# Kernel optimization log

Hardware: AMD Instinct MI355X
Metric: run time of the kernel (lower is better)

Reference implementation:

```python
import jax, jax.numpy as jnp
import numpy as np

NUM_INPUTS = 1024
NUM_HIDDEN = 1024
FORGET_GATE_BIAS = -1.0
EPS = 1e-5


def layer_norm_1d(x, weight, bias):
    # Matches torch LayerNorm1D: std is unbiased (ddof=1), divide by (std + eps)
    mean = jnp.mean(x, axis=1, keepdims=True)
    std = jnp.std(x, axis=1, keepdims=True, ddof=1)
    return (x - mean) / (std + EPS) * weight + bias


def setup_inputs() -> dict:
    key = jax.random.key(0)
    ks = jax.random.split(key, 8)
    B, I, H = 4096, NUM_INPUTS, NUM_HIDDEN
    lim_i = 1.0 / np.sqrt(I)
    lim_h = 1.0 / np.sqrt(H)
    return {
        "inputs": jax.random.normal(ks[0], (B, I), jnp.float32),
        "hx": jax.random.normal(ks[1], (B, H), jnp.float32),
        "cx": jax.random.normal(ks[2], (B, H), jnp.float32),
        "w_i2h": jax.random.uniform(ks[3], (4 * H, I), jnp.float32, -lim_i, lim_i),
        "b_i2h": jax.random.uniform(ks[4], (4 * H,), jnp.float32, -lim_i, lim_i),
        "w_h2h": jax.random.uniform(ks[5], (4 * H, H), jnp.float32, -lim_h, lim_h),
        "b_h2h": jax.random.uniform(ks[6], (4 * H,), jnp.float32, -lim_h, lim_h),
        "ln_i2h_w": jnp.ones((1, 4 * H), jnp.float32),
        "ln_i2h_b": jnp.zeros((1, 4 * H), jnp.float32),
        "ln_h2h_w": jnp.ones((1, 4 * H), jnp.float32),
        "ln_h2h_b": jnp.zeros((1, 4 * H), jnp.float32),
        "ln_h2o_w": jnp.ones((1, H), jnp.float32),
        "ln_h2o_b": jnp.zeros((1, H), jnp.float32),
    }


def reference(inputs, hx, cx, w_i2h, b_i2h, w_h2h, b_h2h,
              ln_i2h_w, ln_i2h_b, ln_h2h_w, ln_h2h_b, ln_h2o_w, ln_h2o_b):
    H = NUM_HIDDEN
    i2h = inputs @ w_i2h.T + b_i2h          # [B, 4H]
    h2h = hx @ w_h2h.T + b_h2h              # [B, 4H]
    x = layer_norm_1d(i2h, ln_i2h_w, ln_i2h_b) + layer_norm_1d(h2h, ln_h2h_w, ln_h2h_b)
    g_i, g_f, g_o, g_c = jnp.split(x, 4, axis=1)
    in_gate = jax.nn.sigmoid(g_i)
    forget_gate = jax.nn.sigmoid(g_f + FORGET_GATE_BIAS)
    out_gate = jax.nn.sigmoid(g_o)
    in_transform = jnp.tanh(g_c)
    cx_new = forget_gate * cx + in_gate * in_transform
    hx_new = out_gate * jnp.tanh(layer_norm_1d(cx_new, ln_h2o_w, ln_h2o_b))
    return hx_new, cx_new
```

## Files before the change

kernel.cpp:

```cpp
#include <hip/hip_runtime.h>
#include <hip/hip_bf16.h>
#include <math.h>

#define NI 1024
#define NH 1024
#define H4 4096
#define FGB (-1.0f)
#define LN_EPS 1e-5f
#define NKT 32

typedef unsigned short u16;
typedef __attribute__((ext_vector_type(8))) short short8;
typedef __attribute__((ext_vector_type(8))) unsigned short ushort8v;
typedef __attribute__((ext_vector_type(16))) float f32x16;

__device__ __forceinline__ float bf2f(u16 u) {
    union { unsigned int i; float f; } v; v.i = ((unsigned int)u) << 16; return v.f;
}
__device__ __forceinline__ u16 f2bf(float f) {
    __hip_bfloat16 h = __float2bfloat16(f);
    return __builtin_bit_cast(u16, h);
}
__device__ __forceinline__ float fast_sigmoid(float x) {
    return 1.0f / (1.0f + __expf(-x));
}
__device__ __forceinline__ float fast_tanh(float x) {
    return 1.0f - 2.0f / (__expf(2.0f * x) + 1.0f);
}

__device__ __forceinline__ void gload16(const u16* g, u16* l) {
    __builtin_amdgcn_global_load_lds(
        (const __attribute__((address_space(1))) void*)g,
        (__attribute__((address_space(3))) void*)l,
        16, 0, 0);
}

__global__ __launch_bounds__(256) void shuffle_cast(
    const float* __restrict__ a, const float* __restrict__ b,
    const float* __restrict__ c, const float* __restrict__ d,
    u16* __restrict__ oa, u16* __restrict__ ob,
    u16* __restrict__ oc, u16* __restrict__ od)
{
    __shared__ u16 sT[32][264];

    const int my = blockIdx.y;
    const float* src = (my == 0) ? a : (my == 1) ? b : (my == 2) ? c : d;
    u16*         dst = (my == 0) ? oa : (my == 1) ? ob : (my == 2) ? oc : od;

    const int mtile = blockIdx.x >> 2;
    const int slab  = blockIdx.x & 3;
    const int t     = threadIdx.x;
    const int w     = t >> 6;
    const int lane  = t & 63;

    const float* s0 = src + (size_t)(mtile * 32) * 1024 + slab * 256 + lane * 4;
#pragma unroll
    for (int i = 0; i < 8; ++i) {
        const int row = i * 4 + w;
        float4 v = *(const float4*)(s0 + (size_t)row * 1024);
        ushort4 pk;
        pk.x = f2bf(v.x); pk.y = f2bf(v.y); pk.z = f2bf(v.z); pk.w = f2bf(v.w);
        *(ushort4*)&sT[row][lane * 4] = pk;
    }
    __syncthreads();

    const int r  = lane & 31;
    const int hi = lane >> 5;
#pragma unroll
    for (int j = 0; j < 2; ++j) {
        const int ktl = w * 2 + j;
        const int kt  = slab * 8 + ktl;
        u16* o = dst + ((size_t)(mtile * 32 + kt)) * 1024 + lane * 8;
#pragma unroll
        for (int kh = 0; kh < 2; ++kh) {
            ushort8v vv = *(const ushort8v*)&sT[r][ktl * 32 + kh * 16 + hi * 8];
            *(ushort8v*)(o + kh * 512) = vv;
        }
    }
}

__global__ __launch_bounds__(512, 2) void gemm_lds(
    const u16* __restrict__ Af0, const u16* __restrict__ Wf0,
    const float* __restrict__ bias0, u16* __restrict__ C0,
    const u16* __restrict__ Af1, const u16* __restrict__ Wf1,
    const float* __restrict__ bias1, u16* __restrict__ C1,
    int N)
{
    const u16*   Af   = blockIdx.z ? Af1 : Af0;
    const u16*   Wf   = blockIdx.z ? Wf1 : Wf0;
    const float* bias = blockIdx.z ? bias1 : bias0;
    u16*         C    = blockIdx.z ? C1 : C0;

    __shared__ __align__(16) u16 sA[4][8][2][512];
    __shared__ __align__(16) u16 sB[4][8][2][512];

    const int tid  = threadIdx.x;
    const int lane = tid & 63;
    const int wave = tid >> 6;
    const int wm   = wave >> 2;
    const int wn   = wave & 3;

    const u16* gA = Af + (size_t)(blockIdx.y * 8 + wave) * 32768 + lane * 8;
    const u16* gB = Wf + (size_t)(blockIdx.x * 8 + wave) * 32768 + lane * 8;

    f32x16 acc[4][2];
#pragma unroll
    for (int i = 0; i < 4; ++i)
#pragma unroll
        for (int j = 0; j < 2; ++j)
#pragma unroll
            for (int r = 0; r < 16; ++r)
                acc[i][j][r] = 0.f;

#define STAGE(kt)                                                            \
    do {                                                                     \
        gload16(gA + (size_t)(kt) * 1024,       &sA[(kt) & 3][wave][0][0]);  \
        gload16(gA + (size_t)(kt) * 1024 + 512, &sA[(kt) & 3][wave][1][0]);  \
        gload16(gB + (size_t)(kt) * 1024,       &sB[(kt) & 3][wave][0][0]);  \
        gload16(gB + (size_t)(kt) * 1024 + 512, &sB[(kt) & 3][wave][1][0]);  \
    } while (0)

    ushort8v a0_0, a1_0, a2_0, a3_0, b0_0, b1_0;
    ushort8v a0_1, a1_1, a2_1, a3_1, b0_1, b1_1;

#define R0(slot)                                                             \
    do {                                                                     \
        a0_0 = *(const ushort8v*)&sA[slot][wm * 4 + 0][0][lane * 8];         \
        b0_0 = *(const ushort8v*)&sB[slot][wn * 2 + 0][0][lane * 8];         \
        a1_0 = *(const ushort8v*)&sA[slot][wm * 4 + 1][0][lane * 8];         \
        b1_0 = *(const ushort8v*)&sB[slot][wn * 2 + 1][0][lane * 8];         \
        a2_0 = *(const ushort8v*)&sA[slot][wm * 4 + 2][0][lane * 8];         \
        a3_0 = *(const ushort8v*)&sA[slot][wm * 4 + 3][0][lane * 8];         \
    } while (0)
#define R1(slot)                                                             \
    do {                                                                     \
        a0_1 = *(const ushort8v*)&sA[slot][wm * 4 + 0][1][lane * 8];         \
        b0_1 = *(const ushort8v*)&sB[slot][wn * 2 + 0][1][lane * 8];         \
        a1_1 = *(const ushort8v*)&sA[slot][wm * 4 + 1][1][lane * 8];         \
        b1_1 = *(const ushort8v*)&sB[slot][wn * 2 + 1][1][lane * 8];         \
        a2_1 = *(const ushort8v*)&sA[slot][wm * 4 + 2][1][lane * 8];         \
        a3_1 = *(const ushort8v*)&sA[slot][wm * 4 + 3][1][lane * 8];         \
    } while (0)

#define MM(i, j, aa, bb) \
    acc[i][j] = __builtin_amdgcn_mfma_f32_32x32x16_bf16((short8)aa, (short8)bb, acc[i][j], 0, 0, 0)

#define M8(s)                                                                \
    do {                                                                     \
        __builtin_amdgcn_s_setprio(1);                                       \
        MM(0, 0, a0_##s, b0_##s); MM(1, 0, a1_##s, b0_##s);                  \
        MM(0, 1, a0_##s, b1_##s); MM(1, 1, a1_##s, b1_##s);                  \
        MM(2, 0, a2_##s, b0_##s); MM(3, 0, a3_##s, b0_##s);                  \
        MM(2, 1, a2_##s, b1_##s); MM(3, 1, a3_##s, b1_##s);                  \
        __builtin_amdgcn_s_setprio(0);                                       \
    } while (0)

#define FENCE() asm volatile("" ::: "memory")
#define WIN_TOP(kt)                                                          \
    do {                                                                     \
        if ((kt) == NKT - 1) {                                               \
            asm volatile("s_waitcnt vmcnt(0)" ::: "memory");                 \
        } else {                                                             \
            asm volatile("s_waitcnt vmcnt(4)" ::: "memory");                 \
        }                                                                    \
        FENCE();                                                             \
        __builtin_amdgcn_s_barrier();                                        \
        FENCE();                                                             \
        if ((kt) + 2 < NKT) STAGE((kt) + 2);                                 \
    } while (0)

    STAGE(0);
    STAGE(1);
    asm volatile("s_waitcnt vmcnt(4)" ::: "memory");
    FENCE();
    __builtin_amdgcn_s_barrier();
    FENCE();
    STAGE(2);
    R0(0);
    R1(0);
    M8(0);

    if ((wave & 1) == 0) {
#pragma unroll
        for (int kt = 1; kt < NKT; ++kt) {
            const int slot = kt & 3;
            WIN_TOP(kt);
            R0(slot);
            M8(1);
            R1(slot);
            M8(0);
        }
    } else {
#pragma unroll
        for (int kt = 1; kt < NKT; ++kt) {
            const int slot = kt & 3;
            WIN_TOP(kt);
            M8(1);
            __builtin_amdgcn_sched_barrier(0);
            R0(slot);
            R1(slot);
            M8(0);
        }
    }
    M8(1);

#undef STAGE
#undef R0
#undef R1
#undef MM
#undef M8
#undef WIN_TOP
#undef FENCE

    const int m0  = blockIdx.y * 256;
    const int n0  = blockIdx.x * 256;
    const int l31 = lane & 31;
    float bv[2];
#pragma unroll
    for (int tn = 0; tn < 2; ++tn)
        bv[tn] = bias[n0 + wn * 64 + tn * 32 + l31];

    const int rbase = (lane >> 5) * 4;
#pragma unroll
    for (int tm = 0; tm < 4; ++tm)
#pragma unroll
        for (int reg = 0; reg < 16; ++reg) {
            const int row = m0 + wm * 128 + tm * 32 + (reg & 3) + 8 * (reg >> 2) + rbase;
#pragma unroll
            for (int tn = 0; tn < 2; ++tn) {
                const int col = n0 + wn * 64 + tn * 32 + l31;
                C[(size_t)row * N + col] = f2bf(acc[tm][tn][reg] + bv[tn]);
            }
        }
}

__global__ __launch_bounds__(256) void lstm_pointwise(
    const u16* __restrict__ i2h, const u16* __restrict__ h2h,
    const float* __restrict__ cx,
    const float* __restrict__ lwx, const float* __restrict__ lbx,
    const float* __restrict__ lwy, const float* __restrict__ lby,
    const float* __restrict__ lwc, const float* __restrict__ lbc,
    float* __restrict__ hx_out, float* __restrict__ cx_out)
{
    __shared__ float red[16];

    const int row  = blockIdx.x;
    const int tid  = threadIdx.x;
    const int lane = tid & 63;
    const int wid  = tid >> 6;
    const int j0   = tid * 4;

    const u16* xr = i2h + (size_t)row * H4;
    const u16* yr = h2h + (size_t)row * H4;

    float xf[4][4], yf[4][4];
    float sx = 0.f, sxx = 0.f, sy = 0.f, syy = 0.f;
#pragma unroll
    for (int g = 0; g < 4; ++g) {
        ushort4 xv = *(const ushort4*)(xr + g * NH + j0);
        ushort4 yv = *(const ushort4*)(yr + g * NH + j0);
        xf[g][0] = bf2f(xv.x); xf[g][1] = bf2f(xv.y);
        xf[g][2] = bf2f(xv.z); xf[g][3] = bf2f(xv.w);
        yf[g][0] = bf2f(yv.x); yf[g][1] = bf2f(yv.y);
        yf[g][2] = bf2f(yv.z); yf[g][3] = bf2f(yv.w);
#pragma unroll
        for (int e = 0; e < 4; ++e) {
            sx += xf[g][e]; sxx += xf[g][e] * xf[g][e];
            sy += yf[g][e]; syy += yf[g][e] * yf[g][e];
        }
    }
#pragma unroll
    for (int m = 32; m; m >>= 1) {
        sx  += __shfl_xor(sx,  m, 64);
        sxx += __shfl_xor(sxx, m, 64);
        sy  += __shfl_xor(sy,  m, 64);
        syy += __shfl_xor(syy, m, 64);
    }
    if (lane == 0) {
        red[wid] = sx; red[4 + wid] = sxx; red[8 + wid] = sy; red[12 + wid] = syy;
    }
    __syncthreads();
    const float tsx  = red[0] + red[1] + red[2] + red[3];
    const float tsxx = red[4] + red[5] + red[6] + red[7];
    const float tsy  = red[8] + red[9] + red[10] + red[11];
    const float tsyy = red[12] + red[13] + red[14] + red[15];

    const float n1  = (float)H4;
    const float mx  = tsx / n1;
    const float ivx = 1.0f / (sqrtf(fmaxf((tsxx - tsx * tsx / n1) / (n1 - 1.f), 0.f)) + LN_EPS);
    const float my  = tsy / n1;
    const float ivy = 1.0f / (sqrtf(fmaxf((tsyy - tsy * tsy / n1) / (n1 - 1.f), 0.f)) + LN_EPS);

    float gate[4][4];
#pragma unroll
    for (int g = 0; g < 4; ++g) {
        float4 wxv = *(const float4*)(lwx + g * NH + j0);
        float4 bxv = *(const float4*)(lbx + g * NH + j0);
        float4 wyv = *(const float4*)(lwy + g * NH + j0);
        float4 byv = *(const float4*)(lby + g * NH + j0);
        gate[g][0] = (xf[g][0] - mx) * ivx * wxv.x + bxv.x + (yf[g][0] - my) * ivy * wyv.x + byv.x;
        gate[g][1] = (xf[g][1] - mx) * ivx * wxv.y + bxv.y + (yf[g][1] - my) * ivy * wyv.y + byv.y;
        gate[g][2] = (xf[g][2] - mx) * ivx * wxv.z + bxv.z + (yf[g][2] - my) * ivy * wyv.z + byv.z;
        gate[g][3] = (xf[g][3] - mx) * ivx * wxv.w + bxv.w + (yf[g][3] - my) * ivy * wyv.w + byv.w;
    }

    float4 cxv = *(const float4*)(cx + (size_t)row * NH + j0);
    const float cin[4] = {cxv.x, cxv.y, cxv.z, cxv.w};
    float cvl[4], og[4];
    float sc = 0.f, scc = 0.f;
#pragma unroll
    for (int e = 0; e < 4; ++e) {
        float ing = fast_sigmoid(gate[0][e]);
        float fg  = fast_sigmoid(gate[1][e] + FGB);
        og[e]     = fast_sigmoid(gate[2][e]);
        float tr  = fast_tanh(gate[3][e]);
        float c   = fg * cin[e] + ing * tr;
        cvl[e] = c; sc += c; scc += c * c;
    }
    *(float4*)(cx_out + (size_t)row * NH + j0) = make_float4(cvl[0], cvl[1], cvl[2], cvl[3]);

#pragma unroll
    for (int m = 32; m; m >>= 1) {
        sc  += __shfl_xor(sc,  m, 64);
        scc += __shfl_xor(scc, m, 64);
    }
    __syncthreads();
    if (lane == 0) { red[wid] = sc; red[4 + wid] = scc; }
    __syncthreads();
    const float tsc  = red[0] + red[1] + red[2] + red[3];
    const float tscc = red[4] + red[5] + red[6] + red[7];

    const float nc  = (float)NH;
    const float mc  = tsc / nc;
    const float ivc = 1.0f / (sqrtf(fmaxf((tscc - tsc * tsc / nc) / (nc - 1.f), 0.f)) + LN_EPS);

    float4 wcv = *(const float4*)(lwc + j0);
    float4 bcv = *(const float4*)(lbc + j0);
    float h0 = og[0] * fast_tanh((cvl[0] - mc) * ivc * wcv.x + bcv.x);
    float h1 = og[1] * fast_tanh((cvl[1] - mc) * ivc * wcv.y + bcv.y);
    float h2 = og[2] * fast_tanh((cvl[2] - mc) * ivc * wcv.z + bcv.z);
    float h3 = og[3] * fast_tanh((cvl[3] - mc) * ivc * wcv.w + bcv.w);
    *(float4*)(hx_out + (size_t)row * NH + j0) = make_float4(h0, h1, h2, h3);
}

extern "C" void kernel_launch(void* const* d_in, const int* in_sizes, int n_in,
                              void* d_out, int out_size, void* d_ws, size_t ws_size,
                              hipStream_t stream) {
    const float* inputs = (const float*)d_in[0];
    const float* hx     = (const float*)d_in[1];
    const float* cx     = (const float*)d_in[2];
    const float* w_i2h  = (const float*)d_in[3];
    const float* b_i2h  = (const float*)d_in[4];
    const float* w_h2h  = (const float*)d_in[5];
    const float* b_h2h  = (const float*)d_in[6];
    const float* lwx    = (const float*)d_in[7];
    const float* lbx    = (const float*)d_in[8];
    const float* lwy    = (const float*)d_in[9];
    const float* lby    = (const float*)d_in[10];
    const float* lwc    = (const float*)d_in[11];
    const float* lbc    = (const float*)d_in[12];

    const int B = in_sizes[0] / NI;

    u16* a_fr   = (u16*)d_ws;
    u16* hx_fr  = a_fr   + (size_t)B * NI;
    u16* wi_fr  = hx_fr  + (size_t)B * NH;
    u16* wh_fr  = wi_fr  + (size_t)H4 * NI;
    u16* i2h_bf = wh_fr  + (size_t)H4 * NH;
    u16* h2h_bf = i2h_bf + (size_t)B * H4;

    float* hx_out = (float*)d_out;
    float* cx_out = hx_out + (size_t)B * NH;

    shuffle_cast<<<dim3(512, 4), dim3(256), 0, stream>>>(
        inputs, hx, w_i2h, w_h2h, a_fr, hx_fr, wi_fr, wh_fr);

    gemm_lds<<<dim3(H4 / 256, B / 256, 2), dim3(512), 0, stream>>>(
        a_fr, wi_fr, b_i2h, i2h_bf,
        hx_fr, wh_fr, b_h2h, h2h_bf,
        H4);

    lstm_pointwise<<<dim3(B), dim3(256), 0, stream>>>(
        i2h_bf, h2h_bf, cx, lwx, lbx, lwy, lby, lwc, lbc, hx_out, cx_out);
}
```

Measured before the change: 237.6 us.

## Restructure GEMM main loop into double-buffered 64-wide K tiles with per-subslice staging

Replaces the 4-slot ring of 32-wide K tiles with a 2-slot buffer of 64-wide K tiles split into four sub-slices. Each sub-slice phase waits on its own load, barriers, reads its fragments, issues the prefetch for the same sub-slice of the next tile, then runs the MFMAs. It also drops the wave-parity split scheduling and the double fragment registers. The aim is finer-grained overlap of global loads with compute and lower register pressure, at the cost of one barrier per 16-wide K step instead of one per 32.

```diff
diff --git a/kernel.cpp b/kernel.cpp
--- a/kernel.cpp
+++ b/kernel.cpp
@@ -8,6 +8,7 @@
 #define FGB (-1.0f)
 #define LN_EPS 1e-5f
 #define NKT 32
+#define NT64 16
 
 typedef unsigned short u16;
 typedef __attribute__((ext_vector_type(8))) short short8;
@@ -91,8 +92,8 @@
     const float* bias = blockIdx.z ? bias1 : bias0;
     u16*         C    = blockIdx.z ? C1 : C0;
 
-    __shared__ __align__(16) u16 sA[4][8][2][512];
-    __shared__ __align__(16) u16 sB[4][8][2][512];
+    __shared__ __align__(16) u16 sA[2][8][4][512];
+    __shared__ __align__(16) u16 sB[2][8][4][512];
 
     const int tid  = threadIdx.x;
     const int lane = tid & 63;
@@ -112,104 +113,72 @@
             for (int r = 0; r < 16; ++r)
                 acc[i][j][r] = 0.f;
 
-#define STAGE(kt)                                                            \
+#define SSUB(t, s)                                                            \
+    do {                                                                      \
+        gload16(gA + (size_t)(t) * 2048 + (s) * 512, &sA[(t) & 1][wave][s][0]); \
+        gload16(gB + (size_t)(t) * 2048 + (s) * 512, &sB[(t) & 1][wave][s][0]); \
+    } while (0)
+
+    ushort8v fa0, fa1, fa2, fa3, fb0, fb1;
+
+#define RD(slot, s)                                                          \
     do {                                                                     \
-        gload16(gA + (size_t)(kt) * 1024,       &sA[(kt) & 3][wave][0][0]);  \
-        gload16(gA + (size_t)(kt) * 1024 + 512, &sA[(kt) & 3][wave][1][0]);  \
-        gload16(gB + (size_t)(kt) * 1024,       &sB[(kt) & 3][wave][0][0]);  \
-        gload16(gB + (size_t)(kt) * 1024 + 512, &sB[(kt) & 3][wave][1][0]);  \
-    } while (0)
-
-    ushort8v a0_0, a1_0, a2_0, a3_0, b0_0, b1_0;
-    ushort8v a0_1, a1_1, a2_1, a3_1, b0_1, b1_1;
-
-#define R0(slot)                                                             \
-    do {                                                                     \
-        a0_0 = *(const ushort8v*)&sA[slot][wm * 4 + 0][0][lane * 8];         \
-        b0_0 = *(const ushort8v*)&sB[slot][wn * 2 + 0][0][lane * 8];         \
-        a1_0 = *(const ushort8v*)&sA[slot][wm * 4 + 1][0][lane * 8];         \
-        b1_0 = *(const ushort8v*)&sB[slot][wn * 2 + 1][0][lane * 8];         \
-        a2_0 = *(const ushort8v*)&sA[slot][wm * 4 + 2][0][lane * 8];         \
-        a3_0 = *(const ushort8v*)&sA[slot][wm * 4 + 3][0][lane * 8];         \
-    } while (0)
-#define R1(slot)                                                             \
-    do {                                                                     \
-        a0_1 = *(const ushort8v*)&sA[slot][wm * 4 + 0][1][lane * 8];         \
-        b0_1 = *(const ushort8v*)&sB[slot][wn * 2 + 0][1][lane * 8];         \
-        a1_1 = *(const ushort8v*)&sA[slot][wm * 4 + 1][1][lane * 8];         \
-        b1_1 = *(const ushort8v*)&sB[slot][wn * 2 + 1][1][lane * 8];         \
-        a2_1 = *(const ushort8v*)&sA[slot][wm * 4 + 2][1][lane * 8];         \
-        a3_1 = *(const ushort8v*)&sA[slot][wm * 4 + 3][1][lane * 8];         \
+        fa0 = *(const ushort8v*)&sA[slot][wm * 4 + 0][s][lane * 8];          \
+        fb0 = *(const ushort8v*)&sB[slot][wn * 2 + 0][s][lane * 8];          \
+        fa1 = *(const ushort8v*)&sA[slot][wm * 4 + 1][s][lane * 8];          \
+        fb1 = *(const ushort8v*)&sB[slot][wn * 2 + 1][s][lane * 8];          \
+        fa2 = *(const ushort8v*)&sA[slot][wm * 4 + 2][s][lane * 8];          \
+        fa3 = *(const ushort8v*)&sA[slot][wm * 4 + 3][s][lane * 8];          \
     } while (0)
 
 #define MM(i, j, aa, bb) \
     acc[i][j] = __builtin_amdgcn_mfma_f32_32x32x16_bf16((short8)aa, (short8)bb, acc[i][j], 0, 0, 0)
 
-#define M8(s)                                                                \
+#define M8()                                                                 \
     do {                                                                     \
         __builtin_amdgcn_s_setprio(1);                                       \
-        MM(0, 0, a0_##s, b0_##s); MM(1, 0, a1_##s, b0_##s);                  \
-        MM(0, 1, a0_##s, b1_##s); MM(1, 1, a1_##s, b1_##s);                  \
-        MM(2, 0, a2_##s, b0_##s); MM(3, 0, a3_##s, b0_##s);                  \
-        MM(2, 1, a2_##s, b1_##s); MM(3, 1, a3_##s, b1_##s);                  \
+        MM(0, 0, fa0, fb0); MM(1, 0, fa1, fb0);                              \
+        MM(0, 1, fa0, fb1); MM(1, 1, fa1, fb1);                              \
+        MM(2, 0, fa2, fb0); MM(3, 0, fa3, fb0);                              \
+        MM(2, 1, fa2, fb1); MM(3, 1, fa3, fb1);                              \
         __builtin_amdgcn_s_setprio(0);                                       \
     } while (0)
 
 #define FENCE() asm volatile("" ::: "memory")
-#define WIN_TOP(kt)                                                          \
+#define WAITVM(n) asm volatile("s_waitcnt vmcnt(" #n ")" ::: "memory")
+#define BAR()                                                                \
+    do { FENCE(); __builtin_amdgcn_s_barrier(); FENCE(); } while (0)
+
+#define PHASE(t, p, WM)                                                      \
     do {                                                                     \
-        if ((kt) == NKT - 1) {                                               \
-            asm volatile("s_waitcnt vmcnt(0)" ::: "memory");                 \
-        } else {                                                             \
-            asm volatile("s_waitcnt vmcnt(4)" ::: "memory");                 \
-        }                                                                    \
-        FENCE();                                                             \
-        __builtin_amdgcn_s_barrier();                                        \
-        FENCE();                                                             \
-        if ((kt) + 2 < NKT) STAGE((kt) + 2);                                 \
+        WAITVM(WM);                                                          \
+        BAR();                                                               \
+        RD((t) & 1, p);                                                      \
+        if ((t) + 1 < NT64) SSUB((t) + 1, p);                                \
+        M8();                                                                \
     } while (0)
 
-    STAGE(0);
-    STAGE(1);
-    asm volatile("s_waitcnt vmcnt(4)" ::: "memory");
-    FENCE();
-    __builtin_amdgcn_s_barrier();
-    FENCE();
-    STAGE(2);
-    R0(0);
-    R1(0);
-    M8(0);
-
-    if ((wave & 1) == 0) {
-#pragma unroll
-        for (int kt = 1; kt < NKT; ++kt) {
-            const int slot = kt & 3;
-            WIN_TOP(kt);
-            R0(slot);
-            M8(1);
-            R1(slot);
-            M8(0);
-        }
-    } else {
-#pragma unroll
-        for (int kt = 1; kt < NKT; ++kt) {
-            const int slot = kt & 3;
-            WIN_TOP(kt);
-            M8(1);
-            __builtin_amdgcn_sched_barrier(0);
-            R0(slot);
-            R1(slot);
-            M8(0);
-        }
-    }
-    M8(1);
-
-#undef STAGE
-#undef R0
-#undef R1
+    SSUB(0, 0); SSUB(0, 1); SSUB(0, 2); SSUB(0, 3);
+
+#pragma unroll
+    for (int t = 0; t < NT64 - 1; ++t) {
+        PHASE(t, 0, 6);
+        PHASE(t, 1, 6);
+        PHASE(t, 2, 6);
+        PHASE(t, 3, 6);
+    }
+    PHASE(NT64 - 1, 0, 6);
+    PHASE(NT64 - 1, 1, 4);
+    PHASE(NT64 - 1, 2, 2);
+    PHASE(NT64 - 1, 3, 0);
+
+#undef SSUB
+#undef RD
 #undef MM
 #undef M8
-#undef WIN_TOP
+#undef PHASE
+#undef WAITVM
+#undef BAR
 #undef FENCE
 
     const int m0  = blockIdx.y * 256;
```

Measured after the change: 242.8 us. 1.02x slower.

## Shrink GEMM block tile to 256x128 with 4 waves and 3-stage LDS ring

Applied to the files above, without the earlier changes.

The GEMM block now runs 256 threads (4 waves) on a 256x128 output tile instead of 512 threads on 256x256. Each wave loads two A fragments plus one B fragment per stage, and the LDS buffer ring drops from 4 slots to 3. The split software pipeline with alternating wave phases is replaced by a single uniform loop: barrier, read from LDS, issue the next prefetch, then 16 MFMAs. Smaller LDS use and more blocks should raise occupancy and grid parallelism, at the cost of lower B reuse per block and less interleaving between MFMAs and LDS reads.

```diff
diff --git a/kernel.cpp b/kernel.cpp
--- a/kernel.cpp
+++ b/kernel.cpp
@@ -79,7 +79,7 @@
     }
 }
 
-__global__ __launch_bounds__(512, 2) void gemm_lds(
+__global__ __launch_bounds__(256, 2) void gemm_lds(
     const u16* __restrict__ Af0, const u16* __restrict__ Wf0,
     const float* __restrict__ bias0, u16* __restrict__ C0,
     const u16* __restrict__ Af1, const u16* __restrict__ Wf1,
@@ -91,17 +91,18 @@
     const float* bias = blockIdx.z ? bias1 : bias0;
     u16*         C    = blockIdx.z ? C1 : C0;
 
-    __shared__ __align__(16) u16 sA[4][8][2][512];
-    __shared__ __align__(16) u16 sB[4][8][2][512];
+    __shared__ __align__(16) u16 sA[3][8][2][512];
+    __shared__ __align__(16) u16 sB[3][4][2][512];
 
     const int tid  = threadIdx.x;
     const int lane = tid & 63;
     const int wave = tid >> 6;
-    const int wm   = wave >> 2;
-    const int wn   = wave & 3;
-
-    const u16* gA = Af + (size_t)(blockIdx.y * 8 + wave) * 32768 + lane * 8;
-    const u16* gB = Wf + (size_t)(blockIdx.x * 8 + wave) * 32768 + lane * 8;
+    const int wm   = wave >> 1;
+    const int wn   = wave & 1;
+
+    const u16* gA0 = Af + (size_t)(blockIdx.y * 8 + wave * 2 + 0) * 32768 + lane * 8;
+    const u16* gA1 = Af + (size_t)(blockIdx.y * 8 + wave * 2 + 1) * 32768 + lane * 8;
+    const u16* gB  = Wf + (size_t)(blockIdx.x * 4 + wave) * 32768 + lane * 8;
 
     f32x16 acc[4][2];
 #pragma unroll
@@ -112,12 +113,15 @@
             for (int r = 0; r < 16; ++r)
                 acc[i][j][r] = 0.f;
 
-#define STAGE(kt)                                                            \
-    do {                                                                     \
-        gload16(gA + (size_t)(kt) * 1024,       &sA[(kt) & 3][wave][0][0]);  \
-        gload16(gA + (size_t)(kt) * 1024 + 512, &sA[(kt) & 3][wave][1][0]);  \
-        gload16(gB + (size_t)(kt) * 1024,       &sB[(kt) & 3][wave][0][0]);  \
-        gload16(gB + (size_t)(kt) * 1024 + 512, &sB[(kt) & 3][wave][1][0]);  \
+#define STAGE(kt)                                                              \
+    do {                                                                       \
+        const int sl_ = (kt) % 3;                                              \
+        gload16(gA0 + (size_t)(kt) * 1024,       &sA[sl_][wave * 2 + 0][0][0]); \
+        gload16(gA0 + (size_t)(kt) * 1024 + 512, &sA[sl_][wave * 2 + 0][1][0]); \
+        gload16(gA1 + (size_t)(kt) * 1024,       &sA[sl_][wave * 2 + 1][0][0]); \
+        gload16(gA1 + (size_t)(kt) * 1024 + 512, &sA[sl_][wave * 2 + 1][1][0]); \
+        gload16(gB  + (size_t)(kt) * 1024,       &sB[sl_][wave][0][0]);         \
+        gload16(gB  + (size_t)(kt) * 1024 + 512, &sB[sl_][wave][1][0]);         \
     } while (0)
 
     ushort8v a0_0, a1_0, a2_0, a3_0, b0_0, b1_0;
@@ -147,73 +151,46 @@
 
 #define M8(s)                                                                \
     do {                                                                     \
-        __builtin_amdgcn_s_setprio(1);                                       \
         MM(0, 0, a0_##s, b0_##s); MM(1, 0, a1_##s, b0_##s);                  \
         MM(0, 1, a0_##s, b1_##s); MM(1, 1, a1_##s, b1_##s);                  \
         MM(2, 0, a2_##s, b0_##s); MM(3, 0, a3_##s, b0_##s);                  \
         MM(2, 1, a2_##s, b1_##s); MM(3, 1, a3_##s, b1_##s);                  \
-        __builtin_amdgcn_s_setprio(0);                                       \
     } while (0)
 
 #define FENCE() asm volatile("" ::: "memory")
-#define WIN_TOP(kt)                                                          \
-    do {                                                                     \
-        if ((kt) == NKT - 1) {                                               \
-            asm volatile("s_waitcnt vmcnt(0)" ::: "memory");                 \
-        } else {                                                             \
-            asm volatile("s_waitcnt vmcnt(4)" ::: "memory");                 \
-        }                                                                    \
-        FENCE();                                                             \
-        __builtin_amdgcn_s_barrier();                                        \
-        FENCE();                                                             \
-        if ((kt) + 2 < NKT) STAGE((kt) + 2);                                 \
-    } while (0)
 
     STAGE(0);
     STAGE(1);
-    asm volatile("s_waitcnt vmcnt(4)" ::: "memory");
-    FENCE();
-    __builtin_amdgcn_s_barrier();
-    FENCE();
-    STAGE(2);
-    R0(0);
-    R1(0);
-    M8(0);
-
-    if ((wave & 1) == 0) {
-#pragma unroll
-        for (int kt = 1; kt < NKT; ++kt) {
-            const int slot = kt & 3;
-            WIN_TOP(kt);
-            R0(slot);
-            M8(1);
-            R1(slot);
-            M8(0);
+
+#pragma unroll
+    for (int kt = 0; kt < NKT; ++kt) {
+        const int slot = kt % 3;
+        if (kt == NKT - 1) {
+            asm volatile("s_waitcnt vmcnt(0)" ::: "memory");
+        } else {
+            asm volatile("s_waitcnt vmcnt(6)" ::: "memory");
         }
-    } else {
-#pragma unroll
-        for (int kt = 1; kt < NKT; ++kt) {
-            const int slot = kt & 3;
-            WIN_TOP(kt);
-            M8(1);
-            __builtin_amdgcn_sched_barrier(0);
-            R0(slot);
-            R1(slot);
-            M8(0);
-        }
-    }
-    M8(1);
+        FENCE();
+        __builtin_amdgcn_s_barrier();
+        FENCE();
+        R0(slot);
+        R1(slot);
+        if (kt + 2 < NKT) STAGE(kt + 2);
+        __builtin_amdgcn_s_setprio(1);
+        M8(0);
+        M8(1);
+        __builtin_amdgcn_s_setprio(0);
+    }
 
 #undef STAGE
 #undef R0
 #undef R1
 #undef MM
 #undef M8
-#undef WIN_TOP
 #undef FENCE
 
     const int m0  = blockIdx.y * 256;
-    const int n0  = blockIdx.x * 256;
+    const int n0  = blockIdx.x * 128;
     const int l31 = lane & 31;
     float bv[2];
 #pragma unroll
@@ -375,7 +352,7 @@
     shuffle_cast<<<dim3(512, 4), dim3(256), 0, stream>>>(
         inputs, hx, w_i2h, w_h2h, a_fr, hx_fr, wi_fr, wh_fr);
 
-    gemm_lds<<<dim3(H4 / 256, B / 256, 2), dim3(512), 0, stream>>>(
+    gemm_lds<<<dim3(H4 / 128, B / 256, 2), dim3(256), 0, stream>>>(
         a_fr, wi_fr, b_i2h, i2h_bf,
         hx_fr, wh_fr, b_h2h, h2h_bf,
         H4);
```

Measured after the change: 245.6 us. +3.3%, slower.
